# Kernel optimization log

Measured on AMD Instinct MI355X. Metric: run time of the kernel, lower is better.

The kernel has to match this reference:

```python
import jax, jax.numpy as jnp
import numpy as np

B, P, D, A = 256, 196, 512, 512

def setup_inputs() -> dict:
    key = jax.random.key(0)
    ks = jax.random.split(key, 12)
    sc = 1.0 / np.sqrt(D)
    sa = 1.0 / np.sqrt(A)
    return {
        "encoder_out": jax.random.normal(ks[0], (B, P, D), jnp.float32),
        "decoder_hidden": jax.random.normal(ks[1], (B, D), jnp.float32),
        "st": jax.random.normal(ks[2], (B, D), jnp.float32),
        "Wv": jax.random.normal(ks[3], (D, A), jnp.float32) * sc,
        "bv": jnp.zeros((A,), jnp.float32),
        "Wh": jax.random.normal(ks[4], (D, A), jnp.float32) * sc,
        "bh": jnp.zeros((A,), jnp.float32),
        "Ws": jax.random.normal(ks[5], (D, A), jnp.float32) * sc,
        "bs": jnp.zeros((A,), jnp.float32),
        "Wav": jax.random.normal(ks[6], (A,), jnp.float32) * sa,
        "bav": jnp.zeros((), jnp.float32),
        "Was": jax.random.normal(ks[7], (A,), jnp.float32) * sa,
        "bas": jnp.zeros((), jnp.float32),
    }

def reference(encoder_out, decoder_hidden, st, Wv, bv, Wh, bh, Ws, bs, Wav, bav, Was, bas):
    # hidden: (B, A)
    hidden = decoder_hidden @ Wh + bh
    # v: (B, P, A)
    v = jnp.einsum('bpd,da->bpa', encoder_out, Wv) + bv
    # z_t: (B, P) -- additive attention scores over pixels
    z_t = jnp.einsum('bpa,a->bp', jnp.tanh(v + hidden[:, None, :]), Wav) + bav
    alpha_t = jax.nn.softmax(z_t, axis=1)
    # c_t: (B, D) -- attention-weighted encoding
    c_t = jnp.einsum('bpd,bp->bd', encoder_out, alpha_t)
    # sentinel branch: s (B, A), s_att (B, 1)
    s = st @ Ws + bs
    s_att = jnp.tanh(s + hidden) @ Was + bas  # (B,)
    z_t_extended = jnp.concatenate([z_t, s_att[:, None]], axis=1)  # (B, P+1)
    alpha_t_hat = jax.nn.softmax(z_t_extended, axis=1)
    beta_t = alpha_t_hat[:, -1:]  # (B, 1)
    c_hat_t = beta_t * st + (1.0 - beta_t) * c_t
    return (c_hat_t, alpha_t, beta_t)
```

## Files before the change

### kernel.cpp

```cpp
#include <hip/hip_runtime.h>
#include <hip/hip_bf16.h>
#include <cstdint>

#define B_ 256
#define P_ 196
#define D_ 512
#define A_ 512

#define OUT_CHAT  0
#define OUT_ALPHA (B_*D_)
#define OUT_BETA  (B_*D_ + B_*P_)

typedef unsigned short ushort_t;
typedef uint32_t u32;
typedef uint64_t u64;
typedef __attribute__((ext_vector_type(8))) __bf16 bf16x8;
typedef __attribute__((ext_vector_type(4))) float f32x4;

__device__ __forceinline__ ushort_t f2bf(float f) {
    union { float f; u32 i; } v; v.f = f;
    u32 r = (v.i + 0x7fffu + ((v.i >> 16) & 1u)) >> 16;
    return (ushort_t)r;
}
__device__ __forceinline__ float bfbits2f(u32 lo16) {
    union { u32 i; float f; } v; v.i = lo16 << 16; return v.f;
}
__device__ __forceinline__ u32 cvt2bf(float x, float y) {
    union { __hip_bfloat162 h; u32 u; } v;
    v.h = __float22bfloat162_rn(make_float2(x, y));
    return v.u;
}
__device__ __forceinline__ float tanh_fast(float x) {
    float e = __expf(2.0f * x);
    return 1.0f - 2.0f / (e + 1.0f);
}
__device__ __forceinline__ void async_load16(const ushort_t* g, ushort_t* l) {
    __builtin_amdgcn_global_load_lds(
        (const __attribute__((address_space(1))) unsigned int*)g,
        (__attribute__((address_space(3))) unsigned int*)l, 16, 0, 0);
}

__global__ __launch_bounds__(256) void k0_all(
    const float* __restrict__ Wv, const float* __restrict__ Wh,
    const float* __restrict__ Ws,
    ushort_t* __restrict__ WvT, ushort_t* __restrict__ WhT,
    ushort_t* __restrict__ WsT)
{
    __shared__ ushort_t tile[32][33];
    const float* W = (blockIdx.z == 0) ? Wv : (blockIdx.z == 1) ? Wh : Ws;
    ushort_t*    WT = (blockIdx.z == 0) ? WvT : (blockIdx.z == 1) ? WhT : WsT;
    int bx = blockIdx.x, by = blockIdx.y;
    int t = threadIdx.x, r = t >> 5, c = t & 31;
#pragma unroll
    for (int i = 0; i < 4; ++i) {
        int row = r + 8 * i;
        tile[row][c] = f2bf(W[(size_t)(by * 32 + row) * A_ + bx * 32 + c]);
    }
    __syncthreads();
#pragma unroll
    for (int i = 0; i < 4; ++i) {
        int row = r + 8 * i;
        WT[(size_t)(bx * 32 + row) * D_ + by * 32 + c] = tile[c][row];
    }
}

__global__ __launch_bounds__(256) void kE_plus(
    const float* __restrict__ E, const float* __restrict__ dh,
    const float* __restrict__ st,
    ushort_t* __restrict__ Ebf, ushort_t* __restrict__ dhbf,
    ushort_t* __restrict__ stbf)
{
    int bx = blockIdx.x;
    if (bx < 12544) {
        size_t i0 = (size_t)bx * 512 + threadIdx.x;
        const float4* src = (const float4*)E;
        u64* dst = (u64*)Ebf;
        float4 v0 = src[i0];
        float4 v1 = src[i0 + 256];
        dst[i0]       = (u64)cvt2bf(v0.x, v0.y) | ((u64)cvt2bf(v0.z, v0.w) << 32);
        dst[i0 + 256] = (u64)cvt2bf(v1.x, v1.y) | ((u64)cvt2bf(v1.z, v1.w) << 32);
    } else {
        int gid = (bx - 12544) * 256 + threadIdx.x;
        float4 dv = ((const float4*)dh)[gid];
        float4 sv = ((const float4*)st)[gid];
        ((u64*)dhbf)[gid] = (u64)cvt2bf(dv.x, dv.y) | ((u64)cvt2bf(dv.z, dv.w) << 32);
        ((u64*)stbf)[gid] = (u64)cvt2bf(sv.x, sv.y) | ((u64)cvt2bf(sv.z, sv.w) << 32);
    }
}

#define PADK 72

__global__ __launch_bounds__(256) void k1_mfma(
    const ushort_t* __restrict__ dhbf, const ushort_t* __restrict__ stbf,
    const ushort_t* __restrict__ WhT,  const ushort_t* __restrict__ WsT,
    const float* __restrict__ bh, const float* __restrict__ bs,
    float* __restrict__ hidden_ws, float* __restrict__ s_ws)
{
    __shared__ ushort_t As[128 * PADK];
    __shared__ ushort_t Bs[128 * PADK];

    int mat = blockIdx.z;
    const ushort_t* Abf = mat ? stbf : dhbf;
    const ushort_t* WT  = mat ? WsT  : WhT;
    const float*    bia = mat ? bs   : bh;
    float*          outp = mat ? s_ws : hidden_ws;

    int tid = threadIdx.x;
    int m0 = blockIdx.y * 128;
    int n0 = blockIdx.x * 128;

    int lane = tid & 63, w = tid >> 6;
    int wm = w & 1, wn = w >> 1;
    int col = lane & 15, q = lane >> 4;

    f32x4 acc[4][4];
#pragma unroll
    for (int tm = 0; tm < 4; ++tm)
#pragma unroll
        for (int tn = 0; tn < 4; ++tn)
            acc[tm][tn] = (f32x4){0.f, 0.f, 0.f, 0.f};

    const ushort_t* arow = As + (wm * 64 + col) * PADK + q * 8;
    const ushort_t* brow = Bs + (wn * 64 + col) * PADK + q * 8;

    int sr = tid >> 3, sc = tid & 7;
    for (int kt = 0; kt < D_ / 64; ++kt) {
#pragma unroll
        for (int i = 0; i < 4; ++i) {
            int row = sr + i * 32;
            *(uint4*)(As + row * PADK + sc * 8) =
                *(const uint4*)(Abf + (size_t)(m0 + row) * D_ + kt * 64 + sc * 8);
            *(uint4*)(Bs + row * PADK + sc * 8) =
                *(const uint4*)(WT + (size_t)(n0 + row) * D_ + kt * 64 + sc * 8);
        }
        __syncthreads();
#pragma unroll
        for (int ks = 0; ks < 2; ++ks) {
            bf16x8 afr[4];
#pragma unroll
            for (int tm = 0; tm < 4; ++tm)
                afr[tm] = *(const bf16x8*)(arow + tm * 16 * PADK + ks * 32);
#pragma unroll
            for (int tn = 0; tn < 4; ++tn) {
                bf16x8 bfr = *(const bf16x8*)(brow + tn * 16 * PADK + ks * 32);
#pragma unroll
                for (int tm = 0; tm < 4; ++tm)
                    acc[tm][tn] = __builtin_amdgcn_mfma_f32_16x16x32_bf16(
                        afr[tm], bfr, acc[tm][tn], 0, 0, 0);
            }
        }
        __syncthreads();
    }

#pragma unroll
    for (int tm = 0; tm < 4; ++tm)
#pragma unroll
        for (int r = 0; r < 4; ++r) {
            int b = m0 + wm * 64 + tm * 16 + q * 4 + r;
#pragma unroll
            for (int tn = 0; tn < 4; ++tn) {
                int n = n0 + wn * 64 + tn * 16 + col;
                outp[(size_t)b * A_ + n] = acc[tm][tn][r] + bia[n];
            }
        }
}

#define BM 128
#define BN 256
#define BKk 64
__global__ __launch_bounds__(256, 3) void k2_z_bf(
    const ushort_t* __restrict__ Ebf, const ushort_t* __restrict__ WvT,
    const float* __restrict__ hidden_ws, const float* __restrict__ bv,
    const float* __restrict__ Wav, float* __restrict__ z2_ws)
{
    __shared__ ushort_t As[BM * BKk];
    __shared__ ushort_t Bs[BN * BKk];
    __shared__ float hv_s[2][BN];
    __shared__ float wav_s[BN];
    __shared__ float zpart[2][BM];

    int tid = threadIdx.x;
    int m0  = blockIdx.x * BM;
    int n0  = blockIdx.y * BN;
    int b0  = m0 / P_;
    int b1  = (m0 + BM - 1) / P_;

    {
        int a = n0 + tid;
        float bva = bv[a];
        hv_s[0][tid] = hidden_ws[(size_t)b0 * A_ + a] + bva;
        hv_s[1][tid] = hidden_ws[(size_t)b1 * A_ + a] + bva;
        wav_s[tid]   = Wav[a];
    }

    int lane = tid & 63, w = tid >> 6;
    int wm = w & 1, wn = w >> 1;
    int col = lane & 15, q = lane >> 4;

    f32x4 acc[4][8];
#pragma unroll
    for (int tm = 0; tm < 4; ++tm)
#pragma unroll
        for (int tn = 0; tn < 8; ++tn)
            acc[tm][tn] = (f32x4){0.f, 0.f, 0.f, 0.f};

    int srow = tid >> 3, spos = tid & 7;
    int gch  = spos ^ (srow & 7);
    const ushort_t* agb = Ebf + (size_t)(m0 + srow) * D_ + gch * 8;
    const ushort_t* bgb = WvT + (size_t)(n0 + srow) * D_ + gch * 8;
    ushort_t* alb = As + tid * 8;
    ushort_t* blb = Bs + tid * 8;

    int fx = col & 7;

    for (int kt = 0; kt < D_ / BKk; ++kt) {
#pragma unroll
        for (int i = 0; i < 4; ++i)
            async_load16(agb + (size_t)i * 32 * D_ + kt * BKk, alb + i * 2048);
#pragma unroll
        for (int i = 0; i < 8; ++i)
            async_load16(bgb + (size_t)i * 32 * D_ + kt * BKk, blb + i * 2048);
        __syncthreads();
#pragma unroll
        for (int ks = 0; ks < 2; ++ks) {
            bf16x8 afr[4];
#pragma unroll
            for (int tm = 0; tm < 4; ++tm)
                afr[tm] = *(const bf16x8*)(As + (wm * 64 + tm * 16 + col) * BKk
                                              + (((ks * 4 + q) ^ fx) * 8));
#pragma unroll
            for (int tn = 0; tn < 8; ++tn) {
                bf16x8 bfr = *(const bf16x8*)(Bs + (wn * 128 + tn * 16 + col) * BKk
                                                 + (((ks * 4 + q) ^ fx) * 8));
#pragma unroll
                for (int tm = 0; tm < 4; ++tm)
                    acc[tm][tn] = __builtin_amdgcn_mfma_f32_16x16x32_bf16(
                        afr[tm], bfr, acc[tm][tn], 0, 0, 0);
            }
        }
        __syncthreads();
    }

#pragma unroll
    for (int tm = 0; tm < 4; ++tm) {
#pragma unroll
        for (int r = 0; r < 4; ++r) {
            int row = wm * 64 + tm * 16 + q * 4 + r;
            int m   = m0 + row;
            int bsel = (m / P_) - b0;
            float zr = 0.f;
#pragma unroll
            for (int tn = 0; tn < 8; ++tn) {
                int nl = wn * 128 + tn * 16 + col;
                zr += wav_s[nl] * tanh_fast(acc[tm][tn][r] + hv_s[bsel][nl]);
            }
#pragma unroll
            for (int msk = 1; msk < 16; msk <<= 1)
                zr += __shfl_xor(zr, msk, 64);
            if (col == 0) zpart[wn][row] = zr;
        }
    }
    __syncthreads();
    if (tid < BM)
        z2_ws[(size_t)blockIdx.y * (B_ * P_) + m0 + tid] =
            zpart[0][tid] + zpart[1][tid];
}

__global__ __launch_bounds__(256) void k3_softmax(
    const float* __restrict__ z2_ws, const float* __restrict__ hidden_ws,
    const float* __restrict__ s_ws, const float* __restrict__ Was,
    const float* __restrict__ bas, const float* __restrict__ bav,
    float* __restrict__ alpha_ws, float* __restrict__ beta_ws,
    float* __restrict__ out)
{
    __shared__ float red[4];
    __shared__ float bm_s, bl_s, sa_s;
    int b = blockIdx.x, t = threadIdx.x;

    {
        int a0 = t, a1 = t + 256;
        float part = Was[a0] * tanh_fast(s_ws[(size_t)b * A_ + a0] + hidden_ws[(size_t)b * A_ + a0])
                   + Was[a1] * tanh_fast(s_ws[(size_t)b * A_ + a1] + hidden_ws[(size_t)b * A_ + a1]);
#pragma unroll
        for (int o = 32; o >= 1; o >>= 1) part += __shfl_down(part, o, 64);
        if ((t & 63) == 0) red[t >> 6] = part;
        __syncthreads();
        if (t == 0) sa_s = red[0] + red[1] + red[2] + red[3] + bas[0];
        __syncthreads();
    }

    float zv = (t < P_) ? (z2_ws[(size_t)b * P_ + t]
                         + z2_ws[(size_t)(B_ * P_) + (size_t)b * P_ + t] + bav[0])
                        : -1e30f;

    float m = zv;
#pragma unroll
    for (int o = 32; o >= 1; o >>= 1) m = fmaxf(m, __shfl_xor(m, o, 64));
    if ((t & 63) == 0) red[t >> 6] = m;
    __syncthreads();
    if (t == 0) bm_s = fmaxf(fmaxf(red[0], red[1]), fmaxf(red[2], red[3]));
    __syncthreads();
    float m1 = bm_s;

    float e = (t < P_) ? __expf(zv - m1) : 0.f;
    float s = e;
#pragma unroll
    for (int o = 32; o >= 1; o >>= 1) s += __shfl_xor(s, o, 64);
    if ((t & 63) == 0) red[t >> 6] = s;
    __syncthreads();
    if (t == 0) bl_s = red[0] + red[1] + red[2] + red[3];
    __syncthreads();
    float l1 = bl_s;

    if (t < P_) {
        float alpha = e / l1;
        alpha_ws[(size_t)b * P_ + t] = alpha;
        out[OUT_ALPHA + (size_t)b * P_ + t] = alpha;
    }
    float sa = sa_s;
    float m2 = fmaxf(m1, sa);
    float l2 = __expf(m1 - m2) * l1 + __expf(sa - m2);
    float beta = __expf(sa - m2) / l2;
    if (t == 0) {
        beta_ws[b] = beta;
        out[OUT_BETA + b] = beta;
    }
}

#define PCH 98
__global__ __launch_bounds__(256) void k4_ct_partial(
    const float* __restrict__ E, const float* __restrict__ alpha_ws,
    float* __restrict__ ctp)
{
    __shared__ float al[PCH];
    int b = blockIdx.x, pc = blockIdx.y, t = threadIdx.x;
    int pbase = pc * PCH;
    if (t < PCH) al[t] = alpha_ws[(size_t)b * P_ + pbase + t];
    __syncthreads();
    const float* eb = E + ((size_t)b * P_ + pbase) * D_ + 2 * t;
    float a0 = 0.f, a1 = 0.f;
#pragma unroll 7
    for (int p = 0; p < PCH; ++p) {
        float2 u = *(const float2*)(eb + (size_t)p * D_);
        float ap = al[p];
        a0 = fmaf(ap, u.x, a0);
        a1 = fmaf(ap, u.y, a1);
    }
    *(float2*)(ctp + ((size_t)pc * B_ + b) * D_ + 2 * t) = make_float2(a0, a1);
}

__global__ __launch_bounds__(256) void k4_combine(
    const float* __restrict__ st, const float* __restrict__ ctp,
    const float* __restrict__ beta_ws, float* __restrict__ out)
{
    int b = blockIdx.x, t = threadIdx.x;
    float beta = beta_ws[b];
    float2 su = *(const float2*)(st + (size_t)b * D_ + 2 * t);
    float2 c0v = *(const float2*)(ctp + (size_t)b * D_ + 2 * t);
    float2 c1v = *(const float2*)(ctp + ((size_t)B_ + b) * D_ + 2 * t);
    float c0 = beta * su.x + (1.f - beta) * (c0v.x + c1v.x);
    float c1 = beta * su.y + (1.f - beta) * (c0v.y + c1v.y);
    *(float2*)(out + (size_t)b * D_ + 2 * t) = make_float2(c0, c1);
}

extern "C" void kernel_launch(void* const* d_in, const int* in_sizes, int n_in,
                              void* d_out, int out_size, void* d_ws, size_t ws_size,
                              hipStream_t stream)
{
    (void)in_sizes; (void)n_in; (void)out_size; (void)ws_size;
    const float* E   = (const float*)d_in[0];
    const float* dh  = (const float*)d_in[1];
    const float* st  = (const float*)d_in[2];
    const float* Wv  = (const float*)d_in[3];
    const float* bv  = (const float*)d_in[4];
    const float* Wh  = (const float*)d_in[5];
    const float* bh  = (const float*)d_in[6];
    const float* Ws  = (const float*)d_in[7];
    const float* bs  = (const float*)d_in[8];
    const float* Wav = (const float*)d_in[9];
    const float* bav = (const float*)d_in[10];
    const float* Was = (const float*)d_in[11];
    const float* bas = (const float*)d_in[12];
    float* out = (float*)d_out;

    char* ws = (char*)d_ws;
    ushort_t* WvT     = (ushort_t*)(ws);
    ushort_t* WhT     = (ushort_t*)(ws + 524288);
    ushort_t* WsT     = (ushort_t*)(ws + 1048576);
    float*    alpha_w = (float*)(ws + 1572864);
    float*    beta_w  = (float*)(ws + 1773568);
    float*    z2_w    = (float*)(ws + 1774592);
    ushort_t* dhbf    = (ushort_t*)(ws + 2176000);
    ushort_t* stbf    = (ushort_t*)(ws + 2438144);
    float*    hidden_w= (float*)(ws + 2700288);
    float*    s_w     = (float*)(ws + 3224576);
    float*    ctp_w   = (float*)(ws + 2700288);
    ushort_t* Ebf     = (ushort_t*)(ws + 3748864);

    k0_all<<<dim3(16, 16, 3), 256, 0, stream>>>(Wv, Wh, Ws, WvT, WhT, WsT);
    kE_plus<<<12544 + 128, 256, 0, stream>>>(E, dh, st, Ebf, dhbf, stbf);
    k1_mfma<<<dim3(4, 2, 2), 256, 0, stream>>>(dhbf, stbf, WhT, WsT, bh, bs,
                                               hidden_w, s_w);
    k2_z_bf<<<dim3((B_ * P_) / BM, A_ / BN), 256, 0, stream>>>(
        Ebf, WvT, hidden_w, bv, Wav, z2_w);
    k3_softmax<<<256, 256, 0, stream>>>(z2_w, hidden_w, s_w, Was, bas, bav,
                                        alpha_w, beta_w, out);
    k4_ct_partial<<<dim3(B_, 2), 256, 0, stream>>>(E, alpha_w, ctp_w);
    k4_combine<<<256, 256, 0, stream>>>(st, ctp_w, beta_w, out);
}
```

Measured before the change: 261.9 us.

## Fuse prep kernels and compute context from bf16 E in one final kernel

Merges the weight transpose/convert kernel into the E/dh/st conversion kernel to save a launch. Replaces the two-pass context partial sum and combine kernels with one kernel that reads the bf16 copy of E, halving the bytes read for the context step and dropping the partial buffer. This trades fp32 precision in c_t for bf16 inputs and halves the grid to 256 blocks, which may reduce memory-level parallelism.

```diff
diff --git a/kernel.cpp b/kernel.cpp
--- a/kernel.cpp
+++ b/kernel.cpp
@@ -40,36 +40,17 @@
         (__attribute__((address_space(3))) unsigned int*)l, 16, 0, 0);
 }
 
-__global__ __launch_bounds__(256) void k0_all(
+__global__ __launch_bounds__(256) void k_prep(
+    const float* __restrict__ E, const float* __restrict__ dh,
+    const float* __restrict__ st,
     const float* __restrict__ Wv, const float* __restrict__ Wh,
     const float* __restrict__ Ws,
+    ushort_t* __restrict__ Ebf, ushort_t* __restrict__ dhbf,
+    ushort_t* __restrict__ stbf,
     ushort_t* __restrict__ WvT, ushort_t* __restrict__ WhT,
     ushort_t* __restrict__ WsT)
 {
     __shared__ ushort_t tile[32][33];
-    const float* W = (blockIdx.z == 0) ? Wv : (blockIdx.z == 1) ? Wh : Ws;
-    ushort_t*    WT = (blockIdx.z == 0) ? WvT : (blockIdx.z == 1) ? WhT : WsT;
-    int bx = blockIdx.x, by = blockIdx.y;
-    int t = threadIdx.x, r = t >> 5, c = t & 31;
-#pragma unroll
-    for (int i = 0; i < 4; ++i) {
-        int row = r + 8 * i;
-        tile[row][c] = f2bf(W[(size_t)(by * 32 + row) * A_ + bx * 32 + c]);
-    }
-    __syncthreads();
-#pragma unroll
-    for (int i = 0; i < 4; ++i) {
-        int row = r + 8 * i;
-        WT[(size_t)(bx * 32 + row) * D_ + by * 32 + c] = tile[c][row];
-    }
-}
-
-__global__ __launch_bounds__(256) void kE_plus(
-    const float* __restrict__ E, const float* __restrict__ dh,
-    const float* __restrict__ st,
-    ushort_t* __restrict__ Ebf, ushort_t* __restrict__ dhbf,
-    ushort_t* __restrict__ stbf)
-{
     int bx = blockIdx.x;
     if (bx < 12544) {
         size_t i0 = (size_t)bx * 512 + threadIdx.x;
@@ -79,12 +60,31 @@
         float4 v1 = src[i0 + 256];
         dst[i0]       = (u64)cvt2bf(v0.x, v0.y) | ((u64)cvt2bf(v0.z, v0.w) << 32);
         dst[i0 + 256] = (u64)cvt2bf(v1.x, v1.y) | ((u64)cvt2bf(v1.z, v1.w) << 32);
-    } else {
+    } else if (bx < 12672) {
         int gid = (bx - 12544) * 256 + threadIdx.x;
         float4 dv = ((const float4*)dh)[gid];
         float4 sv = ((const float4*)st)[gid];
         ((u64*)dhbf)[gid] = (u64)cvt2bf(dv.x, dv.y) | ((u64)cvt2bf(dv.z, dv.w) << 32);
         ((u64*)stbf)[gid] = (u64)cvt2bf(sv.x, sv.y) | ((u64)cvt2bf(sv.z, sv.w) << 32);
+    } else {
+        int idx = bx - 12672;
+        int z   = idx >> 8;
+        int rem = idx & 255;
+        int tby = rem >> 4, tbx = rem & 15;
+        const float* W  = (z == 0) ? Wv  : (z == 1) ? Wh  : Ws;
+        ushort_t*    WT = (z == 0) ? WvT : (z == 1) ? WhT : WsT;
+        int t = threadIdx.x, r = t >> 5, c = t & 31;
+#pragma unroll
+        for (int i = 0; i < 4; ++i) {
+            int row = r + 8 * i;
+            tile[row][c] = f2bf(W[(size_t)(tby * 32 + row) * A_ + tbx * 32 + c]);
+        }
+        __syncthreads();
+#pragma unroll
+        for (int i = 0; i < 4; ++i) {
+            int row = r + 8 * i;
+            WT[(size_t)(tbx * 32 + row) * D_ + tby * 32 + c] = tile[c][row];
+        }
     }
 }
 
@@ -327,39 +327,28 @@
     }
 }
 
-#define PCH 98
-__global__ __launch_bounds__(256) void k4_ct_partial(
-    const float* __restrict__ E, const float* __restrict__ alpha_ws,
-    float* __restrict__ ctp)
-{
-    __shared__ float al[PCH];
-    int b = blockIdx.x, pc = blockIdx.y, t = threadIdx.x;
-    int pbase = pc * PCH;
-    if (t < PCH) al[t] = alpha_ws[(size_t)b * P_ + pbase + t];
-    __syncthreads();
-    const float* eb = E + ((size_t)b * P_ + pbase) * D_ + 2 * t;
+__global__ __launch_bounds__(256) void k4_final(
+    const ushort_t* __restrict__ Ebf, const float* __restrict__ st,
+    const float* __restrict__ alpha_ws, const float* __restrict__ beta_ws,
+    float* __restrict__ out)
+{
+    __shared__ float al[P_];
+    int b = blockIdx.x, t = threadIdx.x;
+    if (t < P_) al[t] = alpha_ws[(size_t)b * P_ + t];
+    __syncthreads();
+    const u32* eb = (const u32*)(Ebf + (size_t)b * P_ * D_) + t;
     float a0 = 0.f, a1 = 0.f;
-#pragma unroll 7
-    for (int p = 0; p < PCH; ++p) {
-        float2 u = *(const float2*)(eb + (size_t)p * D_);
+#pragma unroll 4
+    for (int p = 0; p < P_; ++p) {
+        u32 u = eb[(size_t)p * (D_ / 2)];
         float ap = al[p];
-        a0 = fmaf(ap, u.x, a0);
-        a1 = fmaf(ap, u.y, a1);
-    }
-    *(float2*)(ctp + ((size_t)pc * B_ + b) * D_ + 2 * t) = make_float2(a0, a1);
-}
-
-__global__ __launch_bounds__(256) void k4_combine(
-    const float* __restrict__ st, const float* __restrict__ ctp,
-    const float* __restrict__ beta_ws, float* __restrict__ out)
-{
-    int b = blockIdx.x, t = threadIdx.x;
+        a0 = fmaf(ap, bfbits2f(u & 0xffffu), a0);
+        a1 = fmaf(ap, bfbits2f(u >> 16), a1);
+    }
     float beta = beta_ws[b];
     float2 su = *(const float2*)(st + (size_t)b * D_ + 2 * t);
-    float2 c0v = *(const float2*)(ctp + (size_t)b * D_ + 2 * t);
-    float2 c1v = *(const float2*)(ctp + ((size_t)B_ + b) * D_ + 2 * t);
-    float c0 = beta * su.x + (1.f - beta) * (c0v.x + c1v.x);
-    float c1 = beta * su.y + (1.f - beta) * (c0v.y + c1v.y);
+    float c0 = beta * su.x + (1.f - beta) * a0;
+    float c1 = beta * su.y + (1.f - beta) * a1;
     *(float2*)(out + (size_t)b * D_ + 2 * t) = make_float2(c0, c1);
 }
 
@@ -394,17 +383,15 @@
     ushort_t* stbf    = (ushort_t*)(ws + 2438144);
     float*    hidden_w= (float*)(ws + 2700288);
     float*    s_w     = (float*)(ws + 3224576);
-    float*    ctp_w   = (float*)(ws + 2700288);
     ushort_t* Ebf     = (ushort_t*)(ws + 3748864);
 
-    k0_all<<<dim3(16, 16, 3), 256, 0, stream>>>(Wv, Wh, Ws, WvT, WhT, WsT);
-    kE_plus<<<12544 + 128, 256, 0, stream>>>(E, dh, st, Ebf, dhbf, stbf);
+    k_prep<<<12544 + 128 + 768, 256, 0, stream>>>(E, dh, st, Wv, Wh, Ws,
+                                                  Ebf, dhbf, stbf, WvT, WhT, WsT);
     k1_mfma<<<dim3(4, 2, 2), 256, 0, stream>>>(dhbf, stbf, WhT, WsT, bh, bs,
                                                hidden_w, s_w);
     k2_z_bf<<<dim3((B_ * P_) / BM, A_ / BN), 256, 0, stream>>>(
         Ebf, WvT, hidden_w, bv, Wav, z2_w);
     k3_softmax<<<256, 256, 0, stream>>>(z2_w, hidden_w, s_w, Was, bas, bav,
                                         alpha_w, beta_w, out);
-    k4_ct_partial<<<dim3(B_, 2), 256, 0, stream>>>(E, alpha_w, ctp_w);
-    k4_combine<<<256, 256, 0, stream>>>(st, ctp_w, beta_w, out);
-}
+    k4_final<<<256, 256, 0, stream>>>(Ebf, st, alpha_w, beta_w, out);
+}
```

After: 258.0 us. About the same (-1.5%).
